# Kernel optimization log

Measured on AMD Instinct MI355X. Metric: run time of the kernel, lower is better.

The kernel has to match this reference:

```python
import jax, jax.numpy as jnp
import numpy as np

B, C, H, W = 4, 64, 64, 64
CQK = C // 8


def setup_inputs() -> dict:
    key = jax.random.key(0)
    k0, k1, k2, k3, k4 = jax.random.split(key, 5)
    x = jax.random.normal(k0, (B, C, H, W), dtype=jnp.float32)
    # Conv1d kernel_size=1, bias=False -> plain [out, in] matmul weights
    Wq = jax.random.normal(k1, (CQK, C), dtype=jnp.float32) * 0.05
    Wk = jax.random.normal(k2, (CQK, C), dtype=jnp.float32) * 0.05
    Wv = jax.random.normal(k3, (C, C), dtype=jnp.float32) * 0.05
    # torch init is 0; use a nonzero scalar so the attention path is exercised
    gamma = jax.random.uniform(k4, (1,), dtype=jnp.float32)
    return {"x": x, "Wq": Wq, "Wk": Wk, "Wv": Wv, "gamma": gamma}


def reference(x, Wq, Wk, Wv, gamma):
    shape = x.shape                      # [B, C, H, W]
    xf = x.reshape(shape[0], shape[1], -1)  # [B, C, N]
    q = jnp.einsum('oc,bcn->bon', Wq, xf)   # [B, C/8, N]
    k = jnp.einsum('oc,bcn->bon', Wk, xf)   # [B, C/8, N]
    v = jnp.einsum('oc,bcn->bon', Wv, xf)   # [B, C, N]
    # score[b, n, m] = sum_c q[b, c, n] * k[b, c, m]  (no 1/sqrt(d) scale)
    score = jnp.einsum('bcn,bcm->bnm', q, k)  # [B, N, N]
    # unconventional softmax over dim=1 (rows/first N axis, i.e. per-column)
    score = jax.nn.softmax(score, axis=1)
    out = jnp.einsum('bcn,bnm->bcm', v, score)  # [B, C, N]
    attention = gamma * out + xf
    return attention.reshape(shape)
```

## Files before the change

kernel.cpp:

```cpp
#include <hip/hip_runtime.h>

#define BB 4
#define NN 4096

typedef __attribute__((ext_vector_type(8))) short short8v;
typedef __attribute__((ext_vector_type(4))) short short4v;
typedef __attribute__((ext_vector_type(4))) float float4v;

__device__ __forceinline__ unsigned short f2bf_rn(float f) {
    unsigned u = __float_as_uint(f);
    u += 0x7FFFu + ((u >> 16) & 1u);
    return (unsigned short)(u >> 16);
}

__global__ __launch_bounds__(256) void qkv_kernel(
    const float* __restrict__ x,
    const float* __restrict__ Wq, const float* __restrict__ Wk,
    const float* __restrict__ Wv,
    unsigned short* __restrict__ Qt, unsigned short* __restrict__ Kt,
    unsigned short* __restrict__ Vsw)
{
    __shared__ unsigned short xs[64][68];
    __shared__ unsigned short Ot[64][72];

    const int t    = threadIdx.x;
    const int w    = t >> 6;
    const int lane = t & 63;
    const int quad = lane >> 4;
    const int l15  = lane & 15;
    const int b    = blockIdx.y;
    const int n0   = blockIdx.x * 64;

    #pragma unroll
    for (int i = 0; i < 4; ++i) {
        int c  = (t >> 4) + i * 16;
        int n4 = (t & 15) * 4;
        float4 xv = *(const float4*)&x[(size_t)(b * 64 + c) * NN + n0 + n4];
        short4v pk;
        pk[0] = (short)f2bf_rn(xv.x); pk[1] = (short)f2bf_rn(xv.y);
        pk[2] = (short)f2bf_rn(xv.z); pk[3] = (short)f2bf_rn(xv.w);
        *(short4v*)&xs[c][n4] = pk;
    }

    short8v bw[5][2];
    #pragma unroll
    for (int ot = 0; ot < 5; ++ot) {
        int o = ot * 16 + l15;
        const float* base = (o < 8)  ? (Wq + o * 64)
                           : (o < 16) ? (Wk + (o - 8) * 64)
                                      : (Wv + (o - 16) * 64);
        #pragma unroll
        for (int h = 0; h < 2; ++h) {
            float4 u0 = *(const float4*)&base[h * 32 + quad * 8];
            float4 u1 = *(const float4*)&base[h * 32 + quad * 8 + 4];
            short8v f;
            f[0] = (short)f2bf_rn(u0.x); f[1] = (short)f2bf_rn(u0.y);
            f[2] = (short)f2bf_rn(u0.z); f[3] = (short)f2bf_rn(u0.w);
            f[4] = (short)f2bf_rn(u1.x); f[5] = (short)f2bf_rn(u1.y);
            f[6] = (short)f2bf_rn(u1.z); f[7] = (short)f2bf_rn(u1.w);
            bw[ot][h] = f;
        }
    }
    __syncthreads();

    short8v a0, a1;
    {
        unsigned short* p0 = (unsigned short*)&a0;
        unsigned short* p1 = (unsigned short*)&a1;
        const int nn = w * 16 + l15;
        #pragma unroll
        for (int j = 0; j < 8; ++j) {
            p0[j] = xs[quad * 8 + j][nn];
            p1[j] = xs[32 + quad * 8 + j][nn];
        }
    }

    const float4v zacc = {0.f, 0.f, 0.f, 0.f};
    #pragma unroll
    for (int ot = 0; ot < 5; ++ot) {
        float4v d = __builtin_amdgcn_mfma_f32_16x16x32_bf16(a0, bw[ot][0], zacc, 0, 0, 0);
        d = __builtin_amdgcn_mfma_f32_16x16x32_bf16(a1, bw[ot][1], d, 0, 0, 0);
        if (ot == 0) {
            #pragma unroll
            for (int r = 0; r < 4; ++r) {
                unsigned short v = f2bf_rn(d[r]);
                size_t n = (size_t)(n0 + w * 16 + quad * 4 + r);
                if (l15 < 8) Qt[((size_t)b * NN + n) * 8 + l15] = v;
                else         Kt[((size_t)b * NN + n) * 8 + (l15 - 8)] = v;
            }
        } else {
            short4v pk;
            #pragma unroll
            for (int r = 0; r < 4; ++r) pk[r] = (short)f2bf_rn(d[r]);
            *(short4v*)&Ot[(ot - 1) * 16 + l15][w * 16 + quad * 4] = pk;
        }
    }
    __syncthreads();

    {
        int ci = t >> 5, s = t & 31;
        int ct = ci >> 1, nbl = ci & 1;
        size_t nb = (size_t)blockIdx.x * 2 + nbl;
        unsigned short* cb = Vsw + ((size_t)(b * 4 + ct) * 128 + nb) * 512;
        #pragma unroll
        for (int h = 0; h < 2; ++h) {
            int l = s * 2 + h;
            short8v d = *(short8v*)&Ot[ct * 16 + (l & 15)][nbl * 32 + ((l >> 4) << 3)];
            *(short8v*)(cb + l * 8) = d;
        }
    }
}

__global__ __launch_bounds__(256, 4) void attn_kernel(
    const unsigned short* __restrict__ Qt,
    const unsigned short* __restrict__ Kt,
    const unsigned short* __restrict__ Vsw,
    const float* __restrict__ x, const float* __restrict__ gamma,
    float* __restrict__ out)
{
    __shared__ __align__(16) unsigned short Pb[4][16][40];
    __shared__ float Ored[4][64][17];
    __shared__ float Lred[4][16];
    __shared__ float Lf[16];

    const int t    = threadIdx.x;
    const int w    = t >> 6;
    const int lane = t & 63;
    const int quad = lane >> 4;
    const int l15  = lane & 15;
    const int b    = blockIdx.y;
    const int m0   = blockIdx.x * 16;

    const short8v zfrag = {0, 0, 0, 0, 0, 0, 0, 0};
    const float4v zacc  = {0.f, 0.f, 0.f, 0.f};

    short8v bk = zfrag;
    if (quad == 0)
        bk = *(const short8v*)(Kt + (size_t)(b * NN + m0 + l15) * 8);

    float4v acc[4];
    #pragma unroll
    for (int ct = 0; ct < 4; ++ct) acc[ct] = zacc;
    float Lacc = 0.f;

    const unsigned short* qrow = Qt + (size_t)(b * NN + w * 1024 + l15) * 8;
    const unsigned short* vptr = Vsw + ((size_t)b * 4 * 128 + w * 32) * 512 + lane * 8;

    short8v aq0n = zfrag, aq1n = zfrag;
    if (quad == 0) {
        aq0n = *(const short8v*)(qrow);
        aq1n = *(const short8v*)(qrow + 16 * 8);
    }
    short8v av0n = *(const short8v*)(vptr);
    short8v av1n = *(const short8v*)(vptr + 1 * 128 * 512);
    short8v av2n = *(const short8v*)(vptr + 2 * 128 * 512);
    short8v av3n = *(const short8v*)(vptr + 3 * 128 * 512);

    for (int it = 0; it < 32; ++it) {
        short8v aq0 = aq0n, aq1 = aq1n;
        short8v av0 = av0n, av1 = av1n, av2 = av2n, av3 = av3n;

        const int itn = (it + 1) & 31;
        av0n = *(const short8v*)(vptr + itn * 512);
        av1n = *(const short8v*)(vptr + 1 * 128 * 512 + itn * 512);
        av2n = *(const short8v*)(vptr + 2 * 128 * 512 + itn * 512);
        av3n = *(const short8v*)(vptr + 3 * 128 * 512 + itn * 512);
        if (quad == 0) {
            aq0n = *(const short8v*)(qrow + (size_t)(itn * 32) * 8);
            aq1n = *(const short8v*)(qrow + (size_t)(itn * 32 + 16) * 8);
        }

        float4v s0 = __builtin_amdgcn_mfma_f32_16x16x32_bf16(aq0, bk, zacc, 0, 0, 0);
        float4v s1 = __builtin_amdgcn_mfma_f32_16x16x32_bf16(aq1, bk, zacc, 0, 0, 0);

        float p[8];
        #pragma unroll
        for (int j = 0; j < 4; ++j) p[j]     = __expf(s0[j]);
        #pragma unroll
        for (int j = 0; j < 4; ++j) p[4 + j] = __expf(s1[j]);
        float ps = 0.f;
        #pragma unroll
        for (int j = 0; j < 8; ++j) ps += p[j];
        Lacc += ps;

        short4v pk0, pk1;
        #pragma unroll
        for (int j = 0; j < 4; ++j) {
            pk0[j] = (short)f2bf_rn(p[j]);
            pk1[j] = (short)f2bf_rn(p[4 + j]);
        }
        *(short4v*)&Pb[w][l15][quad * 4]      = pk0;
        *(short4v*)&Pb[w][l15][16 + quad * 4] = pk1;

        short8v bp = *(const short8v*)&Pb[w][l15][quad * 8];

        acc[0] = __builtin_amdgcn_mfma_f32_16x16x32_bf16(av0, bp, acc[0], 0, 0, 0);
        acc[1] = __builtin_amdgcn_mfma_f32_16x16x32_bf16(av1, bp, acc[1], 0, 0, 0);
        acc[2] = __builtin_amdgcn_mfma_f32_16x16x32_bf16(av2, bp, acc[2], 0, 0, 0);
        acc[3] = __builtin_amdgcn_mfma_f32_16x16x32_bf16(av3, bp, acc[3], 0, 0, 0);
    }

    Lacc += __shfl_xor(Lacc, 16, 64);
    Lacc += __shfl_xor(Lacc, 32, 64);
    if (lane < 16) Lred[w][lane] = Lacc;

    #pragma unroll
    for (int ct = 0; ct < 4; ++ct)
        #pragma unroll
        for (int r = 0; r < 4; ++r)
            Ored[w][ct * 16 + quad * 4 + r][l15] = acc[ct][r];
    __syncthreads();

    if (t < 16)
        Lf[t] = 1.f / (Lred[0][t] + Lred[1][t] + Lred[2][t] + Lred[3][t]);
    __syncthreads();

    {
        const float gv = gamma[0];
        int c = t >> 2, m4 = (t & 3) * 4;
        float4 o;
        #pragma unroll
        for (int i = 0; i < 4; ++i) {
            float s = Ored[0][c][m4 + i] + Ored[1][c][m4 + i]
                    + Ored[2][c][m4 + i] + Ored[3][c][m4 + i];
            ((float*)&o)[i] = s * Lf[m4 + i];
        }
        size_t gbase = (size_t)(b * 64 + c) * NN + m0 + m4;
        float4 xv = *(const float4*)&x[gbase];
        float4 r;
        r.x = gv * o.x + xv.x; r.y = gv * o.y + xv.y;
        r.z = gv * o.z + xv.z; r.w = gv * o.w + xv.w;
        *(float4*)&out[gbase] = r;
    }
}

extern "C" void kernel_launch(void* const* d_in, const int* in_sizes, int n_in,
                              void* d_out, int out_size, void* d_ws, size_t ws_size,
                              hipStream_t stream) {
    const float* x     = (const float*)d_in[0];
    const float* Wq    = (const float*)d_in[1];
    const float* Wk    = (const float*)d_in[2];
    const float* Wv    = (const float*)d_in[3];
    const float* gamma = (const float*)d_in[4];
    float* out = (float*)d_out;

    unsigned short* ws = (unsigned short*)d_ws;
    unsigned short* Qt  = ws;
    unsigned short* Kt  = Qt + (size_t)BB * NN * 8;
    unsigned short* Vsw = Kt + (size_t)BB * NN * 8;

    qkv_kernel<<<dim3(NN / 64, BB), 256, 0, stream>>>(x, Wq, Wk, Wv, Qt, Kt, Vsw);
    attn_kernel<<<dim3(NN / 16, BB), 256, 0, stream>>>(Qt, Kt, Vsw, x, gamma, out);
}
```

Before: 96.70 us.

## Switch attention to 32x32x16 MFMA with in-register P transpose via permlane32 swap

The attention kernel moves from 16x16x32 to 32x32x16 bf16 MFMA tiles, with 32 output columns per block and 8 waves. The P matrix is packed with v_cvt_pk_bf16_f32 and redistributed between lane halves with v_permlane32_swap instead of a round trip through shared memory. The V swizzle layout in qkv_kernel changes to match the 32-wide A fragments. The goal is to remove per-iteration LDS traffic and raise MFMA efficiency, at the cost of more registers per thread, a two-phase reduction across wave pairs, and tight coupling to the gfx950 instruction set.

```diff
diff --git a/kernel.cpp b/kernel.cpp
--- a/kernel.cpp
+++ b/kernel.cpp
@@ -6,6 +6,7 @@
 typedef __attribute__((ext_vector_type(8))) short short8v;
 typedef __attribute__((ext_vector_type(4))) short short4v;
 typedef __attribute__((ext_vector_type(4))) float float4v;
+typedef __attribute__((ext_vector_type(16))) float f32x16;
 
 __device__ __forceinline__ unsigned short f2bf_rn(float f) {
     unsigned u = __float_as_uint(f);
@@ -20,8 +21,8 @@
     unsigned short* __restrict__ Qt, unsigned short* __restrict__ Kt,
     unsigned short* __restrict__ Vsw)
 {
-    __shared__ unsigned short xs[64][68];
-    __shared__ unsigned short Ot[64][72];
+    __shared__ __align__(16) unsigned short xs[64][68];
+    __shared__ __align__(16) unsigned short Ot[64][72];
 
     const int t    = threadIdx.x;
     const int w    = t >> 6;
@@ -97,139 +98,145 @@
     }
     __syncthreads();
 
-    {
-        int ci = t >> 5, s = t & 31;
-        int ct = ci >> 1, nbl = ci & 1;
-        size_t nb = (size_t)blockIdx.x * 2 + nbl;
-        unsigned short* cb = Vsw + ((size_t)(b * 4 + ct) * 128 + nb) * 512;
-        #pragma unroll
-        for (int h = 0; h < 2; ++h) {
-            int l = s * 2 + h;
-            short8v d = *(short8v*)&Ot[ct * 16 + (l & 15)][nbl * 32 + ((l >> 4) << 3)];
-            *(short8v*)(cb + l * 8) = d;
-        }
-    }
-}
-
-__global__ __launch_bounds__(256, 4) void attn_kernel(
+    #pragma unroll
+    for (int h = 0; h < 2; ++h) {
+        int ci  = w * 2 + h;
+        int ct  = ci >> 2, nsl = ci & 3;
+        short8v d = *(const short8v*)&Ot[ct * 32 + (lane & 31)][nsl * 16 + ((lane >> 5) << 3)];
+        size_t ns = (size_t)blockIdx.x * 4 + nsl;
+        unsigned short* cb = Vsw + (((size_t)b * 2 + ct) * 256 + ns) * 512;
+        *(short8v*)(cb + lane * 8) = d;
+    }
+}
+
+__global__ __launch_bounds__(512, 4) void attn_kernel(
     const unsigned short* __restrict__ Qt,
     const unsigned short* __restrict__ Kt,
     const unsigned short* __restrict__ Vsw,
     const float* __restrict__ x, const float* __restrict__ gamma,
     float* __restrict__ out)
 {
-    __shared__ __align__(16) unsigned short Pb[4][16][40];
-    __shared__ float Ored[4][64][17];
-    __shared__ float Lred[4][16];
-    __shared__ float Lf[16];
+    __shared__ __align__(16) float Ored[4][64][36];
+    __shared__ __align__(16) float Lred[8][32];
+    __shared__ __align__(16) float Lf[32];
 
     const int t    = threadIdx.x;
     const int w    = t >> 6;
     const int lane = t & 63;
-    const int quad = lane >> 4;
-    const int l15  = lane & 15;
+    const int hi   = lane >> 5;
+    const int l31  = lane & 31;
     const int b    = blockIdx.y;
-    const int m0   = blockIdx.x * 16;
+    const int m0   = blockIdx.x * 32;
 
     const short8v zfrag = {0, 0, 0, 0, 0, 0, 0, 0};
-    const float4v zacc  = {0.f, 0.f, 0.f, 0.f};
+    const f32x16 zero16 = {0.f, 0.f, 0.f, 0.f, 0.f, 0.f, 0.f, 0.f,
+                           0.f, 0.f, 0.f, 0.f, 0.f, 0.f, 0.f, 0.f};
 
     short8v bk = zfrag;
-    if (quad == 0)
-        bk = *(const short8v*)(Kt + (size_t)(b * NN + m0 + l15) * 8);
-
-    float4v acc[4];
-    #pragma unroll
-    for (int ct = 0; ct < 4; ++ct) acc[ct] = zacc;
+    if (!hi) bk = *(const short8v*)(Kt + ((size_t)b * NN + m0 + l31) * 8);
+
+    f32x16 acc0 = zero16, acc1 = zero16;
     float Lacc = 0.f;
 
-    const unsigned short* qrow = Qt + (size_t)(b * NN + w * 1024 + l15) * 8;
-    const unsigned short* vptr = Vsw + ((size_t)b * 4 * 128 + w * 32) * 512 + lane * 8;
-
-    short8v aq0n = zfrag, aq1n = zfrag;
-    if (quad == 0) {
-        aq0n = *(const short8v*)(qrow);
-        aq1n = *(const short8v*)(qrow + 16 * 8);
-    }
-    short8v av0n = *(const short8v*)(vptr);
-    short8v av1n = *(const short8v*)(vptr + 1 * 128 * 512);
-    short8v av2n = *(const short8v*)(vptr + 2 * 128 * 512);
-    short8v av3n = *(const short8v*)(vptr + 3 * 128 * 512);
-
-    for (int it = 0; it < 32; ++it) {
-        short8v aq0 = aq0n, aq1 = aq1n;
-        short8v av0 = av0n, av1 = av1n, av2 = av2n, av3 = av3n;
-
-        const int itn = (it + 1) & 31;
-        av0n = *(const short8v*)(vptr + itn * 512);
-        av1n = *(const short8v*)(vptr + 1 * 128 * 512 + itn * 512);
-        av2n = *(const short8v*)(vptr + 2 * 128 * 512 + itn * 512);
-        av3n = *(const short8v*)(vptr + 3 * 128 * 512 + itn * 512);
-        if (quad == 0) {
-            aq0n = *(const short8v*)(qrow + (size_t)(itn * 32) * 8);
-            aq1n = *(const short8v*)(qrow + (size_t)(itn * 32 + 16) * 8);
-        }
-
-        float4v s0 = __builtin_amdgcn_mfma_f32_16x16x32_bf16(aq0, bk, zacc, 0, 0, 0);
-        float4v s1 = __builtin_amdgcn_mfma_f32_16x16x32_bf16(aq1, bk, zacc, 0, 0, 0);
-
-        float p[8];
-        #pragma unroll
-        for (int j = 0; j < 4; ++j) p[j]     = __expf(s0[j]);
-        #pragma unroll
-        for (int j = 0; j < 4; ++j) p[4 + j] = __expf(s1[j]);
-        float ps = 0.f;
-        #pragma unroll
-        for (int j = 0; j < 8; ++j) ps += p[j];
-        Lacc += ps;
-
-        short4v pk0, pk1;
-        #pragma unroll
-        for (int j = 0; j < 4; ++j) {
-            pk0[j] = (short)f2bf_rn(p[j]);
-            pk1[j] = (short)f2bf_rn(p[4 + j]);
-        }
-        *(short4v*)&Pb[w][l15][quad * 4]      = pk0;
-        *(short4v*)&Pb[w][l15][16 + quad * 4] = pk1;
-
-        short8v bp = *(const short8v*)&Pb[w][l15][quad * 8];
-
-        acc[0] = __builtin_amdgcn_mfma_f32_16x16x32_bf16(av0, bp, acc[0], 0, 0, 0);
-        acc[1] = __builtin_amdgcn_mfma_f32_16x16x32_bf16(av1, bp, acc[1], 0, 0, 0);
-        acc[2] = __builtin_amdgcn_mfma_f32_16x16x32_bf16(av2, bp, acc[2], 0, 0, 0);
-        acc[3] = __builtin_amdgcn_mfma_f32_16x16x32_bf16(av3, bp, acc[3], 0, 0, 0);
-    }
-
-    Lacc += __shfl_xor(Lacc, 16, 64);
+    const unsigned short* qp  = Qt + ((size_t)b * NN + w * 512) * 8;
+    const unsigned short* v0p = Vsw + ((size_t)b * 2 * 256 + w * 32) * 512 + lane * 8;
+    const unsigned short* v1p = v0p + 256 * 512;
+
+    short8v aqn = zfrag;
+    if (!hi) aqn = *(const short8v*)(qp + (size_t)l31 * 8);
+    short8v a00n = *(const short8v*)(v0p);
+    short8v a01n = *(const short8v*)(v0p + 512);
+    short8v a10n = *(const short8v*)(v1p);
+    short8v a11n = *(const short8v*)(v1p + 512);
+
+    for (int it = 0; it < 16; ++it) {
+        short8v aq  = aqn;
+        short8v a00 = a00n, a01 = a01n, a10 = a10n, a11 = a11n;
+
+        const int itn = (it + 1) & 15;
+        a00n = *(const short8v*)(v0p + itn * 1024);
+        a01n = *(const short8v*)(v0p + itn * 1024 + 512);
+        a10n = *(const short8v*)(v1p + itn * 1024);
+        a11n = *(const short8v*)(v1p + itn * 1024 + 512);
+        if (!hi) aqn = *(const short8v*)(qp + (size_t)(itn * 32 + l31) * 8);
+
+        f32x16 s = __builtin_amdgcn_mfma_f32_32x32x16_bf16(aq, bk, zero16, 0, 0, 0);
+
+        float p[16];
+        #pragma unroll
+        for (int j = 0; j < 16; ++j) p[j] = __expf(s[j]);
+        #pragma unroll
+        for (int j = 0; j < 16; ++j) Lacc += p[j];
+
+        unsigned x0, x1, x2, x3, x4, x5, x6, x7;
+        asm("v_cvt_pk_bf16_f32 %0, %1, %2" : "=v"(x0) : "v"(p[0]),  "v"(p[1]));
+        asm("v_cvt_pk_bf16_f32 %0, %1, %2" : "=v"(x1) : "v"(p[2]),  "v"(p[3]));
+        asm("v_cvt_pk_bf16_f32 %0, %1, %2" : "=v"(x2) : "v"(p[4]),  "v"(p[5]));
+        asm("v_cvt_pk_bf16_f32 %0, %1, %2" : "=v"(x3) : "v"(p[6]),  "v"(p[7]));
+        asm("v_cvt_pk_bf16_f32 %0, %1, %2" : "=v"(x4) : "v"(p[8]),  "v"(p[9]));
+        asm("v_cvt_pk_bf16_f32 %0, %1, %2" : "=v"(x5) : "v"(p[10]), "v"(p[11]));
+        asm("v_cvt_pk_bf16_f32 %0, %1, %2" : "=v"(x6) : "v"(p[12]), "v"(p[13]));
+        asm("v_cvt_pk_bf16_f32 %0, %1, %2" : "=v"(x7) : "v"(p[14]), "v"(p[15]));
+
+        asm("v_permlane32_swap_b32 %0, %1" : "+v"(x2), "+v"(x0));
+        asm("v_permlane32_swap_b32 %0, %1" : "+v"(x3), "+v"(x1));
+        asm("v_permlane32_swap_b32 %0, %1" : "+v"(x6), "+v"(x4));
+        asm("v_permlane32_swap_b32 %0, %1" : "+v"(x7), "+v"(x5));
+
+        union { unsigned u[4]; short8v v; } bp0, bp1;
+        bp0.u[0] = x0; bp0.u[1] = x1; bp0.u[2] = x2; bp0.u[3] = x3;
+        bp1.u[0] = x4; bp1.u[1] = x5; bp1.u[2] = x6; bp1.u[3] = x7;
+
+        acc0 = __builtin_amdgcn_mfma_f32_32x32x16_bf16(a00, bp0.v, acc0, 0, 0, 0);
+        acc0 = __builtin_amdgcn_mfma_f32_32x32x16_bf16(a01, bp1.v, acc0, 0, 0, 0);
+        acc1 = __builtin_amdgcn_mfma_f32_32x32x16_bf16(a10, bp0.v, acc1, 0, 0, 0);
+        acc1 = __builtin_amdgcn_mfma_f32_32x32x16_bf16(a11, bp1.v, acc1, 0, 0, 0);
+    }
+
     Lacc += __shfl_xor(Lacc, 32, 64);
-    if (lane < 16) Lred[w][lane] = Lacc;
-
-    #pragma unroll
-    for (int ct = 0; ct < 4; ++ct)
-        #pragma unroll
-        for (int r = 0; r < 4; ++r)
-            Ored[w][ct * 16 + quad * 4 + r][l15] = acc[ct][r];
-    __syncthreads();
-
-    if (t < 16)
-        Lf[t] = 1.f / (Lred[0][t] + Lred[1][t] + Lred[2][t] + Lred[3][t]);
+    if (lane < 32) Lred[w][l31] = Lacc;
+
+    if (w < 4) {
+        #pragma unroll
+        for (int r = 0; r < 16; ++r) {
+            int c = (r & 3) + 8 * (r >> 2) + 4 * hi;
+            Ored[w][c][l31]      = acc0[r];
+            Ored[w][c + 32][l31] = acc1[r];
+        }
+    }
+    __syncthreads();
+    if (w >= 4) {
+        #pragma unroll
+        for (int r = 0; r < 16; ++r) {
+            int c = (r & 3) + 8 * (r >> 2) + 4 * hi;
+            Ored[w - 4][c][l31]      += acc0[r];
+            Ored[w - 4][c + 32][l31] += acc1[r];
+        }
+    }
+    if (t < 32) {
+        float sum = Lred[0][t] + Lred[1][t] + Lred[2][t] + Lred[3][t]
+                  + Lred[4][t] + Lred[5][t] + Lred[6][t] + Lred[7][t];
+        Lf[t] = 1.f / sum;
+    }
     __syncthreads();
 
     {
         const float gv = gamma[0];
-        int c = t >> 2, m4 = (t & 3) * 4;
-        float4 o;
-        #pragma unroll
-        for (int i = 0; i < 4; ++i) {
-            float s = Ored[0][c][m4 + i] + Ored[1][c][m4 + i]
-                    + Ored[2][c][m4 + i] + Ored[3][c][m4 + i];
-            ((float*)&o)[i] = s * Lf[m4 + i];
-        }
-        size_t gbase = (size_t)(b * 64 + c) * NN + m0 + m4;
+        int c = t >> 3, m4 = (t & 7) * 4;
+        float4 o = {0.f, 0.f, 0.f, 0.f};
+        #pragma unroll
+        for (int k2 = 0; k2 < 4; ++k2) {
+            float4 v = *(const float4*)&Ored[k2][c][m4];
+            o.x += v.x; o.y += v.y; o.z += v.z; o.w += v.w;
+        }
+        float4 lf = *(const float4*)&Lf[m4];
+        size_t gbase = ((size_t)b * 64 + c) * NN + m0 + m4;
         float4 xv = *(const float4*)&x[gbase];
         float4 r;
-        r.x = gv * o.x + xv.x; r.y = gv * o.y + xv.y;
-        r.z = gv * o.z + xv.z; r.w = gv * o.w + xv.w;
+        r.x = gv * o.x * lf.x + xv.x;
+        r.y = gv * o.y * lf.y + xv.y;
+        r.z = gv * o.z * lf.z + xv.z;
+        r.w = gv * o.w * lf.w + xv.w;
         *(float4*)&out[gbase] = r;
     }
 }
@@ -250,5 +257,5 @@
     unsigned short* Vsw = Kt + (size_t)BB * NN * 8;
 
     qkv_kernel<<<dim3(NN / 64, BB), 256, 0, stream>>>(x, Wq, Wk, Wv, Qt, Kt, Vsw);
-    attn_kernel<<<dim3(NN / 16, BB), 256, 0, stream>>>(Qt, Kt, Vsw, x, gamma, out);
-}
+    attn_kernel<<<dim3(NN / 32, BB), 512, 0, stream>>>(Qt, Kt, Vsw, x, gamma, out);
+}
```

Result: faster. 86.41 us (-10.6%).
